# Kernel tuning notes

Measured on AMD Instinct MI355X. Metric: run time of the kernel, lower is better.

## Reference

```python
import jax, jax.numpy as jnp
import numpy as np

H = 12  # num_heads

def _attn(q, k, v):
    # q,k,v: [B,H,N,D]; SDPA default scale 1/sqrt(D)
    D = q.shape[-1]
    scores = jnp.einsum('bhnd,bhmd->bhnm', q, k) / jnp.sqrt(jnp.asarray(D, q.dtype))
    p = jax.nn.softmax(scores, axis=-1)
    return jnp.einsum('bhnm,bhmd->bhnd', p, v)

def setup_inputs() -> dict:
    key = jax.random.key(0)
    ks = jax.random.split(key, 5)
    B, N, C = 2, 2048, 768
    s = 0.02
    return {
        'x': jax.random.normal(ks[0], (B, N, C), jnp.float32),
        'Wq': jax.random.normal(ks[1], (C, 2 * C), jnp.float32) * s,
        'Wk': jax.random.normal(ks[2], (C, 2 * C), jnp.float32) * s,
        'Wv': jax.random.normal(ks[3], (C, C), jnp.float32) * s,
        'lambda_p': jnp.zeros((H, 1, 1), jnp.float32),
        'Wo': jax.random.normal(ks[4], (C, C), jnp.float32) * s,
        'bo': jnp.zeros((C,), jnp.float32),
    }

def reference(x, Wq, Wk, Wv, lambda_p, Wo, bo):
    B, N, C = x.shape
    D = C // H
    # [B,N,2C] -> [2,B,H,N,D]
    q = (x @ Wq).reshape(B, N, 2, H, D).transpose(2, 0, 3, 1, 4)
    k = (x @ Wk).reshape(B, N, 2, H, D).transpose(2, 0, 3, 1, 4)
    v = (x @ Wv).reshape(B, N, H, D).transpose(0, 2, 1, 3)
    out1 = _attn(q[0], k[0], v)
    out2 = _attn(q[1], k[1], v)
    lam = jnp.exp(lambda_p)  # [H,1,1] broadcasts over [B,H,N,D]
    out = out1 - lam * out2
    out = out.transpose(0, 2, 1, 3).reshape(B, N, C)
    return out @ Wo + bo
```

## Files before the change

kernel.cpp:

```cpp
#include <hip/hip_runtime.h>

typedef unsigned short u16;
typedef unsigned int u32;
typedef unsigned long long u64;
typedef __bf16 bf16x8 __attribute__((ext_vector_type(8)));
typedef float f32x4 __attribute__((ext_vector_type(4)));
typedef float f32x16 __attribute__((ext_vector_type(16)));

#define B_ 2
#define N_ 2048
#define C_ 768
#define H_ 12
#define M_ 4096
#define SCALE_LOG2 0.18033688011112042f

static __device__ __forceinline__ u16 f2bf(float f) {
  u32 u = __builtin_bit_cast(u32, f);
  u32 r = u + 0x7fffu + ((u >> 16) & 1u);
  return (u16)(r >> 16);
}
static __device__ __forceinline__ float fexp2(float x) {
#if __has_builtin(__builtin_amdgcn_exp2f)
  return __builtin_amdgcn_exp2f(x);
#else
  return __expf(x * 0.6931471805599453f);
#endif
}
static __device__ __forceinline__ u32 pack_bf16(float a, float b) {
  u32 r;
  asm("v_cvt_pk_bf16_f32 %0, %1, %2" : "=v"(r) : "v"(a), "v"(b));
  return r;
}

static __device__ __forceinline__ void gload16(const void* g, void* lds_base) {
  __builtin_amdgcn_global_load_lds(
      (__attribute__((address_space(1))) void*)(u64)(g),
      (__attribute__((address_space(3))) void*)(u32)(u64)(lds_base), 16, 0, 0);
}

__global__ __launch_bounds__(256) void k_cvt4(const float* __restrict__ x,
                                              u16* __restrict__ xb, int n4) {
  int i = blockIdx.x * 256 + threadIdx.x;
  if (i >= n4) return;
  float4 v = ((const float4*)x)[i];
  ushort4 o;
  o.x = f2bf(v.x); o.y = f2bf(v.y); o.z = f2bf(v.z); o.w = f2bf(v.w);
  ((ushort4*)xb)[i] = o;
}

__global__ __launch_bounds__(256) void k_tconv2(const float* __restrict__ W0,
                                                const float* __restrict__ W1,
                                                u16* __restrict__ Wt, int K, int N) {
  const float* W = blockIdx.z ? W1 : W0;
  u16* dst = Wt + (u64)blockIdx.z * N * K;
  __shared__ float t[32][33];
  int n0 = blockIdx.x * 32, k0 = blockIdx.y * 32;
  int tx = threadIdx.x, ty = threadIdx.y;
#pragma unroll
  for (int i = 0; i < 4; i++)
    t[ty + i * 8][tx] = W[(u64)(k0 + ty + i * 8) * N + n0 + tx];
  __syncthreads();
#pragma unroll
  for (int i = 0; i < 4; i++)
    dst[(u64)(n0 + ty + i * 8) * K + k0 + tx] = f2bf(t[tx][ty + i * 8]);
}

__global__ __launch_bounds__(256) void k_gemm_qkv(const u16* __restrict__ A,
                                                  const u16* __restrict__ WQK,
                                                  const u16* __restrict__ WV,
                                                  u16* __restrict__ QKb,
                                                  u16* __restrict__ Vtout) {
  __shared__ u16 As[128 * 32];
  __shared__ u16 Bs[128 * 32];
  const int t = threadIdx.x;
  const int w = t >> 6, l = t & 63;
  const int wr = w >> 1, wc = w & 1;
  const int la = l & 15, lg = l >> 4;
  const int srow = l >> 2, scb = (l & 3) << 4;
  const int by = blockIdx.y;
  const bool isV = by >= 24;

  f32x4 acc[4][4];
#pragma unroll
  for (int i = 0; i < 4; i++)
#pragma unroll
    for (int j = 0; j < 4; j++) acc[i][j] = f32x4{0.f, 0.f, 0.f, 0.f};

  const u16* Ag = A + (u64)(blockIdx.x * 128) * 768;
  const u16* Bg = isV ? WV + (u64)((by - 24) * 128) * 768 : WQK + (u64)(by * 128) * 768;

  for (int k0 = 0; k0 < 768; k0 += 32) {
#pragma unroll
    for (int j = 0; j < 2; j++) {
      int r = (w * 2 + j) * 16 + srow;
      gload16((const char*)(Ag + (u64)r * 768 + k0) + scb, (char*)As + (w * 2 + j) * 1024);
      gload16((const char*)(Bg + (u64)r * 768 + k0) + scb, (char*)Bs + (w * 2 + j) * 1024);
    }
    __syncthreads();
    bf16x8 af[4], bfr[4];
#pragma unroll
    for (int m = 0; m < 4; m++)
      af[m] = *(const bf16x8*)(As + (wr * 64 + m * 16 + la) * 32 + lg * 8);
#pragma unroll
    for (int n = 0; n < 4; n++)
      bfr[n] = *(const bf16x8*)(Bs + (wc * 64 + n * 16 + la) * 32 + lg * 8);
#pragma unroll
    for (int m = 0; m < 4; m++)
#pragma unroll
      for (int n = 0; n < 4; n++)
        acc[m][n] =
            __builtin_amdgcn_mfma_f32_16x16x32_bf16(af[m], bfr[n], acc[m][n], 0, 0, 0);
    __syncthreads();
  }

#pragma unroll
  for (int m = 0; m < 4; m++) {
#pragma unroll
    for (int n = 0; n < 4; n++) {
      int grow0 = blockIdx.x * 128 + wr * 64 + m * 16 + lg * 4;
      if (!isV) {
        int gcol = by * 128 + wc * 64 + n * 16 + la;
        float sc = (gcol < 1536) ? SCALE_LOG2 : 1.0f;
#pragma unroll
        for (int j = 0; j < 4; j++)
          QKb[(u64)(grow0 + j) * 3072 + gcol] = f2bf(acc[m][n][j] * sc);
      } else {
        int gcol = (by - 24) * 128 + wc * 64 + n * 16 + la;
        ushort4 o;
        o.x = f2bf(acc[m][n][0]); o.y = f2bf(acc[m][n][1]);
        o.z = f2bf(acc[m][n][2]); o.w = f2bf(acc[m][n][3]);
        *(ushort4*)(Vtout + (u64)gcol * M_ + grow0) = o;
      }
    }
  }
}

__global__ __launch_bounds__(256) void k_gemm_out(const u16* __restrict__ A,
                                                  const u16* __restrict__ Bt,
                                                  float* __restrict__ Cout,
                                                  const float* __restrict__ bias) {
  __shared__ u16 As[128 * 32];
  __shared__ u16 Bs[128 * 32];
  const int t = threadIdx.x;
  const int w = t >> 6, l = t & 63;
  const int wr = w >> 1, wc = w & 1;
  const int la = l & 15, lg = l >> 4;
  const int srow = l >> 2, scb = (l & 3) << 4;

  f32x4 acc[4][4];
#pragma unroll
  for (int i = 0; i < 4; i++)
#pragma unroll
    for (int j = 0; j < 4; j++) acc[i][j] = f32x4{0.f, 0.f, 0.f, 0.f};

  const u16* Ag = A + (u64)(blockIdx.x * 128) * 768;
  const u16* Bg = Bt + (u64)(blockIdx.y * 128) * 768;

  for (int k0 = 0; k0 < 768; k0 += 32) {
#pragma unroll
    for (int j = 0; j < 2; j++) {
      int r = (w * 2 + j) * 16 + srow;
      gload16((const char*)(Ag + (u64)r * 768 + k0) + scb, (char*)As + (w * 2 + j) * 1024);
      gload16((const char*)(Bg + (u64)r * 768 + k0) + scb, (char*)Bs + (w * 2 + j) * 1024);
    }
    __syncthreads();
    bf16x8 af[4], bfr[4];
#pragma unroll
    for (int m = 0; m < 4; m++)
      af[m] = *(const bf16x8*)(As + (wr * 64 + m * 16 + la) * 32 + lg * 8);
#pragma unroll
    for (int n = 0; n < 4; n++)
      bfr[n] = *(const bf16x8*)(Bs + (wc * 64 + n * 16 + la) * 32 + lg * 8);
#pragma unroll
    for (int m = 0; m < 4; m++)
#pragma unroll
      for (int n = 0; n < 4; n++)
        acc[m][n] =
            __builtin_amdgcn_mfma_f32_16x16x32_bf16(af[m], bfr[n], acc[m][n], 0, 0, 0);
    __syncthreads();
  }

#pragma unroll
  for (int m = 0; m < 4; m++) {
#pragma unroll
    for (int n = 0; n < 4; n++) {
      int grow0 = blockIdx.x * 128 + wr * 64 + m * 16 + lg * 4;
      int gcol = blockIdx.y * 128 + wc * 64 + n * 16 + la;
      float bb = bias[gcol];
#pragma unroll
      for (int j = 0; j < 4; j++)
        Cout[(u64)(grow0 + j) * 768 + gcol] = acc[m][n][j] + bb;
    }
  }
}

__global__ __launch_bounds__(256, 3) void k_attn6(const u16* __restrict__ QKb,
                                                  const u16* __restrict__ Vt,
                                                  const float* __restrict__ lamp,
                                                  u16* __restrict__ Ob) {
  const int hw = blockIdx.x;
  const int wid = (hw & 7) * 96 + (hw >> 3);
  const int qt = wid & 31;
  const int hb = wid >> 5;
  const int h = hb % H_, b = hb / H_;

  __shared__ __align__(16) char smem[32768];
  char* ks0 = smem;
  char* ks1 = smem + 8192;
  const int t = threadIdx.x, w = t >> 6, l = t & 63;
  const int p = w >> 1, s = w & 1;
  const int ql = l & 31, hh = l >> 5;
  char* pw = smem + 16384 + w * 4096;
  const int swq = (ql & 7) << 4;

  const u16* qrow =
      QKb + (u64)(b * N_ + qt * 64 + s * 32 + ql) * 3072 + p * 768 + h * 64 + hh * 8;
  bf16x8 qf[4];
#pragma unroll
  for (int c = 0; c < 4; c++) qf[c] = *(const bf16x8*)(qrow + 16 * c);

  f32x16 oacc0, oacc1;
#pragma unroll
  for (int r = 0; r < 16; r++) { oacc0[r] = 0.f; oacc1[r] = 0.f; }
  float l_run = 0.f;

  const int rA = t >> 3, cbs = (t & 7) << 4;
  const u32 swA = (u32)(rA * 128 + (cbs ^ ((rA & 7) << 4)));
  const char* kg = (const char*)(QKb + (u64)(b * N_ + rA) * 3072 + 1536 + h * 64) + cbs;
  const u64 KR32 = (u64)32 * 3072 * 2;
  const u64 KSTEP = (u64)64 * 3072 * 2;

  const char* vb0 = (const char*)(Vt + (u64)(h * 64 + ql) * M_ + b * N_) + 16 * hh;
  const char* vb1 = (const char*)(Vt + (u64)(h * 64 + 32 + ql) * M_ + b * N_) + 16 * hh;
  u32 kvb = 0;

  uint4 rk0A, rk0B, rk1A, rk1B;
#define LOADS4()                              \
  do {                                        \
    rk0A = *(const uint4*)(kg);               \
    rk0B = *(const uint4*)(kg + KR32);        \
    rk1A = *(const uint4*)(kg + 1536);        \
    rk1B = *(const uint4*)(kg + 1536 + KR32); \
  } while (0)
  LOADS4();

  const char* ksp = p ? ks1 : ks0;
  int koff[4];
#pragma unroll
  for (int c = 0; c < 4; c++) koff[c] = (32 * c + 16 * hh) ^ swq;

  for (int kt = 0; kt < 32; kt++) {
    asm volatile("s_waitcnt vmcnt(0)" ::: "memory");
    __builtin_amdgcn_sched_barrier(0);
    *(uint4*)(ks0 + swA) = rk0A;
    *(uint4*)(ks0 + swA + 4096) = rk0B;
    *(uint4*)(ks1 + swA) = rk1A;
    *(uint4*)(ks1 + swA + 4096) = rk1B;
    asm volatile("s_waitcnt lgkmcnt(0)" ::: "memory");
    __builtin_amdgcn_s_barrier();

    bf16x8 vf0[4];
#pragma unroll
    for (int c = 0; c < 4; c++) vf0[c] = *(const bf16x8*)(vb0 + kvb + 32 * c);
    kg += KSTEP;
    if (kt < 31) LOADS4();
    __builtin_amdgcn_sched_barrier(0);

    f32x16 st0, st1;
#pragma unroll
    for (int r = 0; r < 16; r++) { st0[r] = 0.f; st1[r] = 0.f; }
    __builtin_amdgcn_s_setprio(1);
#pragma unroll
    for (int c = 0; c < 4; c++) {
      bf16x8 kf0 = *(const bf16x8*)(ksp + ql * 128 + koff[c]);
      bf16x8 kf1 = *(const bf16x8*)(ksp + (32 + ql) * 128 + koff[c]);
      st0 = __builtin_amdgcn_mfma_f32_32x32x16_bf16(kf0, qf[c], st0, 0, 0, 0);
      st1 = __builtin_amdgcn_mfma_f32_32x32x16_bf16(kf1, qf[c], st1, 0, 0, 0);
    }
    __builtin_amdgcn_s_setprio(0);

    bf16x8 vf1[4];
#pragma unroll
    for (int c = 0; c < 4; c++) vf1[c] = *(const bf16x8*)(vb1 + kvb + 32 * c);

#pragma unroll
    for (int r = 0; r < 16; r++) {
      st0[r] = fexp2(st0[r]);
      st1[r] = fexp2(st1[r]);
    }
    float sm[16];
#pragma unroll
    for (int r = 0; r < 16; r++) sm[r] = st0[r] + st1[r];
#pragma unroll
    for (int sd = 8; sd >= 1; sd >>= 1)
#pragma unroll
      for (int r = 0; r < sd; r++) sm[r] += sm[r + sd];
    l_run += sm[0] + __shfl_xor(sm[0], 32, 64);

#pragma unroll
    for (int g = 0; g < 4; g++) {
      uint2 w0, w1;
      w0.x = pack_bf16(st0[4 * g + 0], st0[4 * g + 1]);
      w0.y = pack_bf16(st0[4 * g + 2], st0[4 * g + 3]);
      w1.x = pack_bf16(st1[4 * g + 0], st1[4 * g + 1]);
      w1.y = pack_bf16(st1[4 * g + 2], st1[4 * g + 3]);
      int bo = 16 * g + 8 * hh;
      *(uint2*)(pw + ql * 128 + (bo ^ swq)) = w0;
      *(uint2*)(pw + ql * 128 + ((64 + bo) ^ swq)) = w1;
    }
    bf16x8 pa[4];
#pragma unroll
    for (int c = 0; c < 4; c++)
      pa[c] = *(const bf16x8*)(pw + ql * 128 + koff[c]);

    __builtin_amdgcn_s_setprio(1);
#pragma unroll
    for (int c = 0; c < 4; c++)
      oacc0 = __builtin_amdgcn_mfma_f32_32x32x16_bf16(pa[c], vf0[c], oacc0, 0, 0, 0);
#pragma unroll
    for (int c = 0; c < 4; c++)
      oacc1 = __builtin_amdgcn_mfma_f32_32x32x16_bf16(pa[c], vf1[c], oacc1, 0, 0, 0);
    __builtin_amdgcn_s_setprio(0);
    __builtin_amdgcn_s_barrier();
    kvb += 128;
  }

  float inv = 1.f / l_run;
  float iT[16];
#pragma unroll
  for (int r = 0; r < 16; r++)
    iT[r] = __shfl(inv, (r & 3) + 8 * (r >> 2) + 4 * hh, 64);
  float* cmb = (float*)smem;
  __syncthreads();
  if (p == 1) {
    float lam = __expf(lamp[h]);
#pragma unroll
    for (int r = 0; r < 16; r++) {
      int qr = (r & 3) + 8 * (r >> 2) + 4 * hh;
      cmb[(s * 32 + qr) * 64 + ql] = lam * oacc0[r] * iT[r];
      cmb[(s * 32 + qr) * 64 + 32 + ql] = lam * oacc1[r] * iT[r];
    }
  }
  __syncthreads();
  if (p == 0) {
    u16* Og = Ob + (u64)(b * N_ + qt * 64 + s * 32) * C_ + h * 64;
#pragma unroll
    for (int r = 0; r < 16; r++) {
      int qr = (r & 3) + 8 * (r >> 2) + 4 * hh;
      float v0 = oacc0[r] * iT[r] - cmb[(s * 32 + qr) * 64 + ql];
      float v1 = oacc1[r] * iT[r] - cmb[(s * 32 + qr) * 64 + 32 + ql];
      Og[(u64)qr * C_ + ql] = f2bf(v0);
      Og[(u64)qr * C_ + 32 + ql] = f2bf(v1);
    }
  }
}

extern "C" void kernel_launch(void* const* d_in, const int* in_sizes, int n_in,
                              void* d_out, int out_size, void* d_ws, size_t ws_size,
                              hipStream_t stream) {
  const float* x = (const float*)d_in[0];
  const float* Wq = (const float*)d_in[1];
  const float* Wk = (const float*)d_in[2];
  const float* Wv = (const float*)d_in[3];
  const float* lamp = (const float*)d_in[4];
  const float* Wo = (const float*)d_in[5];
  const float* bo = (const float*)d_in[6];

  char* ws = (char*)d_ws;
  u16* xb = (u16*)ws;    ws += (u64)M_ * C_ * 2;
  u16* wqkt = (u16*)ws;  ws += (u64)4 * C_ * C_ * 2;
  u16* wvo = (u16*)ws;   ws += (u64)2 * C_ * C_ * 2;
  u16* QKb = (u16*)ws;   ws += (u64)M_ * 4 * C_ * 2;
  u16* Vt = (u16*)ws;    ws += (u64)C_ * M_ * 2;
  u16* Ob = (u16*)ws;    ws += (u64)M_ * C_ * 2;
  u16* wvt = wvo;
  u16* wot = wvo + (u64)C_ * C_;

  k_cvt4<<<dim3(M_ * C_ / 4 / 256), 256, 0, stream>>>(x, xb, M_ * C_ / 4);
  k_tconv2<<<dim3(48, 24, 2), dim3(32, 8), 0, stream>>>(Wq, Wk, wqkt, 768, 1536);
  k_tconv2<<<dim3(24, 24, 2), dim3(32, 8), 0, stream>>>(Wv, Wo, wvo, 768, 768);
  k_gemm_qkv<<<dim3(32, 30), 256, 0, stream>>>(xb, wqkt, wvt, QKb, Vt);
  k_attn6<<<dim3(768), 256, 0, stream>>>(QKb, Vt, lamp, Ob);
  k_gemm_out<<<dim3(32, 6), 256, 0, stream>>>(Ob, wot, (float*)d_out, bo);
}
```

Measured before the change: 177.0 us.

## Split attention KV tile across wave pairs and stage V through padded LDS

The attention kernel now assigns each wave both 32-row query halves and half of each 64-key tile, instead of one query half and the full key tile. V is staged through shared memory alongside K, in padded-stride layouts (136/72 byte strides) that replace XOR swizzling. Partial outputs and row sums from the two key halves are merged through LDS at the end. This is meant to let waves reuse K/V fragments across two query blocks and cut redundant global V reads. In exchange it uses more registers (launch bounds drop to 2 blocks), more LDS, and adds extra reduction barriers.

```diff
diff --git a/kernel.cpp b/kernel.cpp
--- a/kernel.cpp
+++ b/kernel.cpp
@@ -14,6 +14,13 @@
 #define M_ 4096
 #define SCALE_LOG2 0.18033688011112042f
 
+#define KSTR 136
+#define PSTR 72
+#define K1OFF 8704
+#define VOFF 17408
+#define POFF 26112
+#define PWSZ 2304
+
 static __device__ __forceinline__ u16 f2bf(float f) {
   u32 u = __builtin_bit_cast(u32, f);
   u32 r = u + 0x7fffu + ((u >> 16) & 1u);
@@ -30,6 +37,10 @@
   u32 r;
   asm("v_cvt_pk_bf16_f32 %0, %1, %2" : "=v"(r) : "v"(a), "v"(b));
   return r;
+}
+static __device__ __forceinline__ bf16x8 mk8(uint2 a, uint2 b) {
+  uint4 u = make_uint4(a.x, a.y, b.x, b.y);
+  return __builtin_bit_cast(bf16x8, u);
 }
 
 static __device__ __forceinline__ void gload16(const void* g, void* lds_base) {
@@ -194,7 +205,7 @@
   }
 }
 
-__global__ __launch_bounds__(256, 3) void k_attn6(const u16* __restrict__ QKb,
+__global__ __launch_bounds__(256, 2) void k_attn7(const u16* __restrict__ QKb,
                                                   const u16* __restrict__ Vt,
                                                   const float* __restrict__ lamp,
                                                   u16* __restrict__ Ob) {
@@ -204,154 +215,202 @@
   const int hb = wid >> 5;
   const int h = hb % H_, b = hb / H_;
 
-  __shared__ __align__(16) char smem[32768];
-  char* ks0 = smem;
-  char* ks1 = smem + 8192;
+  __shared__ __align__(16) char smem[35328];
   const int t = threadIdx.x, w = t >> 6, l = t & 63;
-  const int p = w >> 1, s = w & 1;
+  const int p = w >> 1, kvh = w & 1;
   const int ql = l & 31, hh = l >> 5;
-  char* pw = smem + 16384 + w * 4096;
-  const int swq = (ql & 7) << 4;
-
-  const u16* qrow =
-      QKb + (u64)(b * N_ + qt * 64 + s * 32 + ql) * 3072 + p * 768 + h * 64 + hh * 8;
-  bf16x8 qf[4];
-#pragma unroll
-  for (int c = 0; c < 4; c++) qf[c] = *(const bf16x8*)(qrow + 16 * c);
-
-  f32x16 oacc0, oacc1;
-#pragma unroll
-  for (int r = 0; r < 16; r++) { oacc0[r] = 0.f; oacc1[r] = 0.f; }
-  float l_run = 0.f;
-
-  const int rA = t >> 3, cbs = (t & 7) << 4;
-  const u32 swA = (u32)(rA * 128 + (cbs ^ ((rA & 7) << 4)));
-  const char* kg = (const char*)(QKb + (u64)(b * N_ + rA) * 3072 + 1536 + h * 64) + cbs;
+
+  bf16x8 qf[2][4];
+#pragma unroll
+  for (int s = 0; s < 2; s++) {
+    const u16* qrow =
+        QKb + (u64)(b * N_ + qt * 64 + s * 32 + ql) * 3072 + p * 768 + h * 64 + hh * 8;
+#pragma unroll
+    for (int c = 0; c < 4; c++) qf[s][c] = *(const bf16x8*)(qrow + 16 * c);
+  }
+
+  f32x16 oacc[2][2];
+#pragma unroll
+  for (int s = 0; s < 2; s++)
+#pragma unroll
+    for (int dh = 0; dh < 2; dh++)
+#pragma unroll
+      for (int r = 0; r < 16; r++) oacc[s][dh][r] = 0.f;
+  float l_run[2] = {0.f, 0.f};
+
+  const int rA = t >> 3, cb = (t & 7) << 4;
+  const char* kg = (const char*)(QKb + (u64)(b * N_ + rA) * 3072 + 1536 + h * 64) + cb;
+  const char* vg = (const char*)(Vt + (u64)(h * 64 + rA) * M_ + b * N_) + cb;
   const u64 KR32 = (u64)32 * 3072 * 2;
+  const u64 VR32 = (u64)32 * M_ * 2;
   const u64 KSTEP = (u64)64 * 3072 * 2;
-
-  const char* vb0 = (const char*)(Vt + (u64)(h * 64 + ql) * M_ + b * N_) + 16 * hh;
-  const char* vb1 = (const char*)(Vt + (u64)(h * 64 + 32 + ql) * M_ + b * N_) + 16 * hh;
-  u32 kvb = 0;
-
-  uint4 rk0A, rk0B, rk1A, rk1B;
-#define LOADS4()                              \
+  char* d0a = smem + rA * KSTR + cb;
+  char* d0b = smem + (rA + 32) * KSTR + cb;
+
+  uint4 rk0A, rk0B, rk1A, rk1B, rvA, rvB;
+#define LOADS6()                              \
   do {                                        \
     rk0A = *(const uint4*)(kg);               \
     rk0B = *(const uint4*)(kg + KR32);        \
     rk1A = *(const uint4*)(kg + 1536);        \
     rk1B = *(const uint4*)(kg + 1536 + KR32); \
+    rvA = *(const uint4*)(vg);                \
+    rvB = *(const uint4*)(vg + VR32);         \
   } while (0)
-  LOADS4();
-
-  const char* ksp = p ? ks1 : ks0;
-  int koff[4];
-#pragma unroll
-  for (int c = 0; c < 4; c++) koff[c] = (32 * c + 16 * hh) ^ swq;
+  LOADS6();
+
+  const char* kbase = smem + p * K1OFF + (32 * kvh + ql) * KSTR + 16 * hh;
+  const char* vb0 = smem + VOFF + ql * KSTR + 64 * kvh + 16 * hh;
+  const char* vb1 = smem + VOFF + (32 + ql) * KSTR + 64 * kvh + 16 * hh;
+  char* pb = smem + POFF + w * PWSZ;
+  char* pwr = pb + ql * PSTR + 8 * hh;
+  const char* prd = pb + ql * PSTR + 16 * hh;
 
   for (int kt = 0; kt < 32; kt++) {
     asm volatile("s_waitcnt vmcnt(0)" ::: "memory");
     __builtin_amdgcn_sched_barrier(0);
-    *(uint4*)(ks0 + swA) = rk0A;
-    *(uint4*)(ks0 + swA + 4096) = rk0B;
-    *(uint4*)(ks1 + swA) = rk1A;
-    *(uint4*)(ks1 + swA + 4096) = rk1B;
+    *(uint2*)(d0a) = make_uint2(rk0A.x, rk0A.y);
+    *(uint2*)(d0a + 8) = make_uint2(rk0A.z, rk0A.w);
+    *(uint2*)(d0b) = make_uint2(rk0B.x, rk0B.y);
+    *(uint2*)(d0b + 8) = make_uint2(rk0B.z, rk0B.w);
+    *(uint2*)(d0a + K1OFF) = make_uint2(rk1A.x, rk1A.y);
+    *(uint2*)(d0a + K1OFF + 8) = make_uint2(rk1A.z, rk1A.w);
+    *(uint2*)(d0b + K1OFF) = make_uint2(rk1B.x, rk1B.y);
+    *(uint2*)(d0b + K1OFF + 8) = make_uint2(rk1B.z, rk1B.w);
+    *(uint2*)(d0a + VOFF) = make_uint2(rvA.x, rvA.y);
+    *(uint2*)(d0a + VOFF + 8) = make_uint2(rvA.z, rvA.w);
+    *(uint2*)(d0b + VOFF) = make_uint2(rvB.x, rvB.y);
+    *(uint2*)(d0b + VOFF + 8) = make_uint2(rvB.z, rvB.w);
     asm volatile("s_waitcnt lgkmcnt(0)" ::: "memory");
     __builtin_amdgcn_s_barrier();
-
-    bf16x8 vf0[4];
-#pragma unroll
-    for (int c = 0; c < 4; c++) vf0[c] = *(const bf16x8*)(vb0 + kvb + 32 * c);
     kg += KSTEP;
-    if (kt < 31) LOADS4();
+    vg += 128;
+    if (kt < 31) LOADS6();
     __builtin_amdgcn_sched_barrier(0);
 
-    f32x16 st0, st1;
-#pragma unroll
-    for (int r = 0; r < 16; r++) { st0[r] = 0.f; st1[r] = 0.f; }
-    __builtin_amdgcn_s_setprio(1);
-#pragma unroll
-    for (int c = 0; c < 4; c++) {
-      bf16x8 kf0 = *(const bf16x8*)(ksp + ql * 128 + koff[c]);
-      bf16x8 kf1 = *(const bf16x8*)(ksp + (32 + ql) * 128 + koff[c]);
-      st0 = __builtin_amdgcn_mfma_f32_32x32x16_bf16(kf0, qf[c], st0, 0, 0, 0);
-      st1 = __builtin_amdgcn_mfma_f32_32x32x16_bf16(kf1, qf[c], st1, 0, 0, 0);
-    }
-    __builtin_amdgcn_s_setprio(0);
-
-    bf16x8 vf1[4];
-#pragma unroll
-    for (int c = 0; c < 4; c++) vf1[c] = *(const bf16x8*)(vb1 + kvb + 32 * c);
-
-#pragma unroll
-    for (int r = 0; r < 16; r++) {
-      st0[r] = fexp2(st0[r]);
-      st1[r] = fexp2(st1[r]);
-    }
-    float sm[16];
-#pragma unroll
-    for (int r = 0; r < 16; r++) sm[r] = st0[r] + st1[r];
-#pragma unroll
-    for (int sd = 8; sd >= 1; sd >>= 1)
-#pragma unroll
-      for (int r = 0; r < sd; r++) sm[r] += sm[r + sd];
-    l_run += sm[0] + __shfl_xor(sm[0], 32, 64);
-
-#pragma unroll
-    for (int g = 0; g < 4; g++) {
-      uint2 w0, w1;
-      w0.x = pack_bf16(st0[4 * g + 0], st0[4 * g + 1]);
-      w0.y = pack_bf16(st0[4 * g + 2], st0[4 * g + 3]);
-      w1.x = pack_bf16(st1[4 * g + 0], st1[4 * g + 1]);
-      w1.y = pack_bf16(st1[4 * g + 2], st1[4 * g + 3]);
-      int bo = 16 * g + 8 * hh;
-      *(uint2*)(pw + ql * 128 + (bo ^ swq)) = w0;
-      *(uint2*)(pw + ql * 128 + ((64 + bo) ^ swq)) = w1;
-    }
-    bf16x8 pa[4];
+    bf16x8 kf[4];
 #pragma unroll
     for (int c = 0; c < 4; c++)
-      pa[c] = *(const bf16x8*)(pw + ql * 128 + koff[c]);
-
-    __builtin_amdgcn_s_setprio(1);
-#pragma unroll
-    for (int c = 0; c < 4; c++)
-      oacc0 = __builtin_amdgcn_mfma_f32_32x32x16_bf16(pa[c], vf0[c], oacc0, 0, 0, 0);
-#pragma unroll
-    for (int c = 0; c < 4; c++)
-      oacc1 = __builtin_amdgcn_mfma_f32_32x32x16_bf16(pa[c], vf1[c], oacc1, 0, 0, 0);
-    __builtin_amdgcn_s_setprio(0);
+      kf[c] = mk8(*(const uint2*)(kbase + 32 * c), *(const uint2*)(kbase + 32 * c + 8));
+    bf16x8 vf[2][2];
+#pragma unroll
+    for (int dh = 0; dh < 2; dh++) {
+      const char* vb = dh ? vb1 : vb0;
+#pragma unroll
+      for (int c2 = 0; c2 < 2; c2++)
+        vf[dh][c2] =
+            mk8(*(const uint2*)(vb + 32 * c2), *(const uint2*)(vb + 32 * c2 + 8));
+    }
+
+#pragma unroll
+    for (int s = 0; s < 2; s++) {
+      f32x16 st;
+#pragma unroll
+      for (int r = 0; r < 16; r++) st[r] = 0.f;
+      __builtin_amdgcn_s_setprio(1);
+#pragma unroll
+      for (int c = 0; c < 4; c++)
+        st = __builtin_amdgcn_mfma_f32_32x32x16_bf16(kf[c], qf[s][c], st, 0, 0, 0);
+      __builtin_amdgcn_s_setprio(0);
+
+      float sm[16];
+#pragma unroll
+      for (int r = 0; r < 16; r++) {
+        st[r] = fexp2(st[r]);
+        sm[r] = st[r];
+      }
+#pragma unroll
+      for (int sd = 8; sd >= 1; sd >>= 1)
+#pragma unroll
+        for (int r = 0; r < sd; r++) sm[r] += sm[r + sd];
+      l_run[s] += sm[0] + __shfl_xor(sm[0], 32, 64);
+
+#pragma unroll
+      for (int g = 0; g < 4; g++) {
+        uint2 pk;
+        pk.x = pack_bf16(st[4 * g + 0], st[4 * g + 1]);
+        pk.y = pack_bf16(st[4 * g + 2], st[4 * g + 3]);
+        *(uint2*)(pwr + 16 * g) = pk;
+      }
+      bf16x8 pa[2];
+#pragma unroll
+      for (int c2 = 0; c2 < 2; c2++)
+        pa[c2] =
+            mk8(*(const uint2*)(prd + 32 * c2), *(const uint2*)(prd + 32 * c2 + 8));
+
+      __builtin_amdgcn_s_setprio(1);
+#pragma unroll
+      for (int c2 = 0; c2 < 2; c2++)
+#pragma unroll
+        for (int dh = 0; dh < 2; dh++)
+          oacc[s][dh] = __builtin_amdgcn_mfma_f32_32x32x16_bf16(pa[c2], vf[dh][c2],
+                                                                oacc[s][dh], 0, 0, 0);
+      __builtin_amdgcn_s_setprio(0);
+    }
     __builtin_amdgcn_s_barrier();
-    kvb += 128;
-  }
-
-  float inv = 1.f / l_run;
-  float iT[16];
-#pragma unroll
-  for (int r = 0; r < 16; r++)
-    iT[r] = __shfl(inv, (r & 3) + 8 * (r >> 2) + 4 * hh, 64);
-  float* cmb = (float*)smem;
+  }
+
+  float* Os = (float*)smem;
+  float* lsc = (float*)(smem + 32768);
   __syncthreads();
-  if (p == 1) {
+  if (kvh == 1) {
+#pragma unroll
+    for (int s = 0; s < 2; s++) {
+#pragma unroll
+      for (int dh = 0; dh < 2; dh++)
+#pragma unroll
+        for (int r = 0; r < 16; r++) {
+          int q = s * 32 + (r & 3) + 8 * (r >> 2) + 4 * hh;
+          Os[(p * 64 + q) * 64 + dh * 32 + ql] = oacc[s][dh][r];
+        }
+      lsc[p * 64 + s * 32 + ql] = l_run[s];
+    }
+  }
+  __syncthreads();
+  if (kvh == 0) {
+#pragma unroll
+    for (int s = 0; s < 2; s++) {
+#pragma unroll
+      for (int dh = 0; dh < 2; dh++)
+#pragma unroll
+        for (int r = 0; r < 16; r++) {
+          int q = s * 32 + (r & 3) + 8 * (r >> 2) + 4 * hh;
+          oacc[s][dh][r] += Os[(p * 64 + q) * 64 + dh * 32 + ql];
+        }
+      l_run[s] += lsc[p * 64 + s * 32 + ql];
+    }
+  }
+  __syncthreads();
+  if (kvh == 0 && p == 1) {
     float lam = __expf(lamp[h]);
-#pragma unroll
-    for (int r = 0; r < 16; r++) {
-      int qr = (r & 3) + 8 * (r >> 2) + 4 * hh;
-      cmb[(s * 32 + qr) * 64 + ql] = lam * oacc0[r] * iT[r];
-      cmb[(s * 32 + qr) * 64 + 32 + ql] = lam * oacc1[r] * iT[r];
-    }
+    float inv[2] = {lam / l_run[0], lam / l_run[1]};
+#pragma unroll
+    for (int s = 0; s < 2; s++)
+#pragma unroll
+      for (int dh = 0; dh < 2; dh++)
+#pragma unroll
+        for (int r = 0; r < 16; r++) {
+          int qm = (r & 3) + 8 * (r >> 2) + 4 * hh;
+          float iT = __shfl(inv[s], qm, 64);
+          Os[(64 + s * 32 + qm) * 64 + dh * 32 + ql] = oacc[s][dh][r] * iT;
+        }
   }
   __syncthreads();
-  if (p == 0) {
-    u16* Og = Ob + (u64)(b * N_ + qt * 64 + s * 32) * C_ + h * 64;
-#pragma unroll
-    for (int r = 0; r < 16; r++) {
-      int qr = (r & 3) + 8 * (r >> 2) + 4 * hh;
-      float v0 = oacc0[r] * iT[r] - cmb[(s * 32 + qr) * 64 + ql];
-      float v1 = oacc1[r] * iT[r] - cmb[(s * 32 + qr) * 64 + 32 + ql];
-      Og[(u64)qr * C_ + ql] = f2bf(v0);
-      Og[(u64)qr * C_ + 32 + ql] = f2bf(v1);
-    }
+  if (kvh == 0 && p == 0) {
+    float inv[2] = {1.f / l_run[0], 1.f / l_run[1]};
+    u16* Og = Ob + (u64)(b * N_ + qt * 64) * C_ + h * 64;
+#pragma unroll
+    for (int s = 0; s < 2; s++)
+#pragma unroll
+      for (int dh = 0; dh < 2; dh++)
+#pragma unroll
+        for (int r = 0; r < 16; r++) {
+          int qm = (r & 3) + 8 * (r >> 2) + 4 * hh;
+          float iT = __shfl(inv[s], qm, 64);
+          int q = s * 32 + qm, d = dh * 32 + ql;
+          float v = oacc[s][dh][r] * iT - Os[(64 + q) * 64 + d];
+          Og[(u64)q * C_ + d] = f2bf(v);
+        }
   }
 }
 
@@ -380,6 +439,6 @@
   k_tconv2<<<dim3(48, 24, 2), dim3(32, 8), 0, stream>>>(Wq, Wk, wqkt, 768, 1536);
   k_tconv2<<<dim3(24, 24, 2), dim3(32, 8), 0, stream>>>(Wv, Wo, wvo, 768, 768);
   k_gemm_qkv<<<dim3(32, 30), 256, 0, stream>>>(xb, wqkt, wvt, QKb, Vt);
-  k_attn6<<<dim3(768), 256, 0, stream>>>(QKb, Vt, lamp, Ob);
+  k_attn7<<<dim3(768), 256, 0, stream>>>(QKb, Vt, lamp, Ob);
   k_gemm_out<<<dim3(32, 6), 256, 0, stream>>>(Ob, wot, (float*)d_out, bo);
 }
```

Measured after the change: 150.6 us. 1.18x faster.
